# Optimization experiments

Measured on AMD Instinct MI355X. Metric: run time of the kernel, lower is better.

The kernel has to match this reference:

```python
import jax, jax.numpy as jnp
import numpy as np

K = 2            # negative:positive edge ratio (init arg k)
N_NODES = 4096
N_EDGES = 8192
FEAT = 64


def setup_inputs() -> dict:
    key = jax.random.key(0)
    k1, k2, k3 = jax.random.split(key, 3)
    node_feature = jax.random.normal(k1, (N_NODES, FEAT), dtype=jnp.float32)
    edge_src = jax.random.randint(k2, (N_EDGES,), 0, N_NODES, dtype=jnp.int32)
    edge_dst = jax.random.randint(k3, (N_EDGES,), 0, N_NODES, dtype=jnp.int32)
    return {"node_feature": node_feature, "edge_src": edge_src, "edge_dst": edge_dst}


def reference(node_feature, edge_src, edge_dst):
    E = edge_src.shape[0]
    N = node_feature.shape[0]
    # [E, E] pairwise mask: candidate column j is valid for row i iff
    # dst[j] != dst[i] and dst[j] != src[i]
    valid = (edge_dst[:, None] != edge_dst[None, :]) & (edge_src[:, None] != edge_dst[None, :])
    # unsorted_segment_min over rows grouped by edge_src -> [N, E]
    segmin = jax.ops.segment_min(valid.astype(jnp.int8), edge_src, num_segments=N)
    # gather back per edge -> [E, E], flatten
    m = segmin[edge_src].reshape(-1).astype(bool)  # [E*E]
    num_negatives = jnp.sum(m)
    ratio = num_negatives // E                      # integer ratio as in TF code
    keep_prob = (K / ratio).astype(jnp.float32)
    u = jax.random.uniform(jax.random.key(42), (E * E,), dtype=jnp.float32)
    keep = m & (u < keep_prob)
    # fixed-size (jit-friendly) stand-in for tf.boolean_mask: expected count is K*E;
    # pad/truncate to exactly K*E kept flat indices (fill_value=0 pads).
    idx = jnp.nonzero(keep, size=K * E, fill_value=0)[0]
    rows = idx // E
    cols = idx % E
    edge_src_neg = edge_src[rows]
    edge_dst_neg = edge_dst[cols]
    return edge_src_neg, edge_dst_neg
```

## Files before the change

kernel.cpp:

```cpp
#include <hip/hip_runtime.h>
#include <stdint.h>

typedef unsigned int u32;
typedef unsigned long long u64;

#define E_CNT   8192
#define N_CNT   4096
#define TOT_N   (1u << 26)
#define OUT_K   16384
#define NODE_BM_WORDS 128
#define N_CHUNKS 1024

#define OFF_BAD      0x000000
#define OFF_CNT_DST  0x200000
#define OFF_CNT_SRC  0x204000
#define OFF_CCOUNT   0x208000
#define OFF_COFF     0x209000
#define OFF_SCALARS  0x20A000
#define OFF_KEEPBM   0x210000
#define ZERO_BYTES   0x20A100

__device__ __forceinline__ u32 rotl32(u32 x, u32 d) { return (x << d) | (x >> (32u - d)); }

__device__ __forceinline__ void threefry_0_42(u32 x0, u32 x1, u32& o0, u32& o1) {
  const u32 k0 = 0u, k1 = 42u, k2 = 0x1BD11BF0u;
  x0 += k0; x1 += k1;
#define TF_R(r) { x0 += x1; x1 = rotl32(x1, r); x1 ^= x0; }
  TF_R(13) TF_R(15) TF_R(26) TF_R(6)
  x0 += k1; x1 += k2 + 1u;
  TF_R(17) TF_R(29) TF_R(16) TF_R(24)
  x0 += k2; x1 += k0 + 2u;
  TF_R(13) TF_R(15) TF_R(26) TF_R(6)
  x0 += k0; x1 += k1 + 3u;
  TF_R(17) TF_R(29) TF_R(16) TF_R(24)
  x0 += k1; x1 += k2 + 4u;
  TF_R(13) TF_R(15) TF_R(26) TF_R(6)
  x0 += k2; x1 += k0 + 5u;
#undef TF_R
  o0 = x0; o1 = x1;
}

__device__ __forceinline__ float bits_to_unif(u32 b) {
  return __uint_as_float((b >> 9) | 0x3f800000u) - 1.0f;
}

__global__ void k_build(const int* __restrict__ src, const int* __restrict__ dst,
                        u32* __restrict__ bad, u32* __restrict__ cnt_dst,
                        u32* __restrict__ cnt_src) {
  int tid = blockIdx.x * 256 + threadIdx.x;
  if (tid < N_CNT) {
    atomicOr(&bad[(u32)tid * NODE_BM_WORDS + ((u32)tid >> 5)], 1u << (tid & 31));
  }
  if (tid < E_CNT) {
    u32 s = (u32)src[tid], d = (u32)dst[tid];
    atomicOr(&bad[s * NODE_BM_WORDS + (d >> 5)], 1u << (d & 31));
    atomicAdd(&cnt_dst[d], 1u);
    atomicAdd(&cnt_src[s], 1u);
  }
}

__global__ void k_rowcount(const u32* __restrict__ bad, const u32* __restrict__ cnt_dst,
                           const u32* __restrict__ cnt_src, u32* __restrict__ num_neg) {
  int n = blockIdx.x * 256 + threadIdx.x;
  u32 sum = 0;
  const u32* row = bad + (u32)n * NODE_BM_WORDS;
  for (int w = 0; w < NODE_BM_WORDS; ++w) {
    u32 bits = row[w];
    while (bits) { int b = __ffs(bits) - 1; sum += cnt_dst[w * 32 + b]; bits &= bits - 1; }
  }
  u32 contrib = ((u32)E_CNT - sum) * cnt_src[n];
  __shared__ u32 red[256];
  red[threadIdx.x] = contrib; __syncthreads();
  for (int off = 128; off > 0; off >>= 1) {
    if (threadIdx.x < off) red[threadIdx.x] += red[threadIdx.x + off];
    __syncthreads();
  }
  if (threadIdx.x == 0) atomicAdd(num_neg, red[0]);
}

__global__ void k_prob(const u32* __restrict__ num_neg, float* __restrict__ kp) {
  u32 ratio = num_neg[0] / (u32)E_CNT;
  kp[0] = 2.0f / (float)ratio;
}

__global__ void __launch_bounds__(256) k_sample(const int* __restrict__ src,
                                                const int* __restrict__ dst,
                                                const u32* __restrict__ bad,
                                                const float* __restrict__ kp_p,
                                                u64* __restrict__ keep_bm,
                                                u32* __restrict__ ccount) {
  u32 i = blockIdx.x * 256u + threadIdx.x;
  u32 o0, o1;
  threefry_0_42(0u, i, o0, o1);
  float u = bits_to_unif(o0 ^ o1);
  float kp = kp_p[0];
  bool keep = u < kp;
  if (keep) {
    u32 n = (u32)src[i >> 13]; u32 v = (u32)dst[i & 8191];
    keep = ((bad[n * NODE_BM_WORDS + (v >> 5)] >> (v & 31)) & 1u) == 0u;
  }
  u64 m = __ballot(keep);
  if ((threadIdx.x & 63) == 0) {
    keep_bm[i >> 6] = m;
    if (m) atomicAdd(&ccount[i >> 16], (u32)__popcll(m));
  }
}

__global__ void k_scan(const u32* __restrict__ ccount, u32* __restrict__ coff) {
  __shared__ u32 s[N_CHUNKS];
  int t = threadIdx.x;
  u32 mine = ccount[t];
  s[t] = mine; __syncthreads();
  for (int off = 1; off < N_CHUNKS; off <<= 1) {
    u32 v = (t >= off) ? s[t - off] : 0u;
    __syncthreads();
    s[t] += v;
    __syncthreads();
  }
  coff[t] = s[t] - mine;
}

__global__ void k_prefill(const int* __restrict__ src, const int* __restrict__ dst,
                          int* __restrict__ out) {
  int r = blockIdx.x * 256 + threadIdx.x;
  out[r] = src[0];
  out[OUT_K + r] = dst[0];
}

__global__ void k_compact(const int* __restrict__ src, const int* __restrict__ dst,
                          const u64* __restrict__ keep_bm, const u32* __restrict__ coff,
                          int* __restrict__ out) {
  int c = blockIdx.x;
  const u64* words = keep_bm + (size_t)c * 1024;
  int t = threadIdx.x;
  u64 w[4];
  u32 cnt = 0;
#pragma unroll
  for (int k = 0; k < 4; ++k) { w[k] = words[4 * t + k]; cnt += (u32)__popcll(w[k]); }
  __shared__ u32 s[256];
  s[t] = cnt; __syncthreads();
  for (int off = 1; off < 256; off <<= 1) {
    u32 v = (t >= off) ? s[t - off] : 0u;
    __syncthreads();
    s[t] += v;
    __syncthreads();
  }
  u32 rank = coff[c] + s[t] - cnt;
  u32 tbase = (u32)c * 65536u + (u32)t * 256u;
#pragma unroll
  for (int k = 0; k < 4; ++k) {
    u64 bits = w[k];
    while (bits) {
      int b = __ffsll((unsigned long long)bits) - 1;
      if (rank < OUT_K) {
        u32 tt = tbase + (u32)k * 64u + (u32)b;
        out[rank]         = src[tt >> 13];
        out[OUT_K + rank] = dst[tt & 8191];
      }
      rank++;
      bits &= bits - 1;
    }
  }
}

extern "C" void kernel_launch(void* const* d_in, const int* in_sizes, int n_in,
                              void* d_out, int out_size, void* d_ws, size_t ws_size,
                              hipStream_t stream) {
  const int* src = (const int*)d_in[1];
  const int* dst = (const int*)d_in[2];
  int* out = (int*)d_out;
  char* ws = (char*)d_ws;

  u32*   bad     = (u32*)(ws + OFF_BAD);
  u32*   cnt_dst = (u32*)(ws + OFF_CNT_DST);
  u32*   cnt_src = (u32*)(ws + OFF_CNT_SRC);
  u32*   ccount  = (u32*)(ws + OFF_CCOUNT);
  u32*   coff    = (u32*)(ws + OFF_COFF);
  u32*   num_neg = (u32*)(ws + OFF_SCALARS);
  float* kp      = (float*)(ws + OFF_SCALARS + 4);
  u64*   keep_bm = (u64*)(ws + OFF_KEEPBM);

  hipMemsetAsync(ws, 0, ZERO_BYTES, stream);
  k_build<<<(E_CNT + 255) / 256, 256, 0, stream>>>(src, dst, bad, cnt_dst, cnt_src);
  k_rowcount<<<N_CNT / 256, 256, 0, stream>>>(bad, cnt_dst, cnt_src, num_neg);
  k_prob<<<1, 1, 0, stream>>>(num_neg, kp);
  k_sample<<<TOT_N / 256, 256, 0, stream>>>(src, dst, bad, kp, keep_bm, ccount);
  k_scan<<<1, N_CHUNKS, 0, stream>>>(ccount, coff);
  k_prefill<<<OUT_K / 256, 256, 0, stream>>>(src, dst, out);
  k_compact<<<N_CHUNKS, 256, 0, stream>>>(src, dst, keep_bm, coff, out);
}
```

Before: 228.1 us.

## Fuse small kernels: prefill into build, prob into rowcount, scan into compact

Cuts the launch chain from seven kernels to four. The output prefill now happens in k_build, and the keep-probability is computed by the last block of k_rowcount through a completion counter. Each k_compact block redoes the 1024-chunk prefix scan redundantly. k_rowcount now uses one wavefront per node with a shuffle reduction, and k_sample compares integer random bits against a precomputed threshold instead of converting to float. These changes remove launch gaps and tiny serial kernels, at the cost of redundant scan work and relying on the threshold comparison being exactly equivalent to the float one.

```diff
diff --git a/kernel.cpp b/kernel.cpp
--- a/kernel.cpp
+++ b/kernel.cpp
@@ -1,5 +1,6 @@
 #include <hip/hip_runtime.h>
 #include <stdint.h>
+#include <math.h>
 
 typedef unsigned int u32;
 typedef unsigned long long u64;
@@ -15,10 +16,9 @@
 #define OFF_CNT_DST  0x200000
 #define OFF_CNT_SRC  0x204000
 #define OFF_CCOUNT   0x208000
-#define OFF_COFF     0x209000
-#define OFF_SCALARS  0x20A000
+#define OFF_SCALARS  0x209000
 #define OFF_KEEPBM   0x210000
-#define ZERO_BYTES   0x20A100
+#define ZERO_BYTES   0x209040
 
 __device__ __forceinline__ u32 rotl32(u32 x, u32 d) { return (x << d) | (x >> (32u - d)); }
 
@@ -40,61 +40,61 @@
   o0 = x0; o1 = x1;
 }
 
-__device__ __forceinline__ float bits_to_unif(u32 b) {
-  return __uint_as_float((b >> 9) | 0x3f800000u) - 1.0f;
-}
-
 __global__ void k_build(const int* __restrict__ src, const int* __restrict__ dst,
                         u32* __restrict__ bad, u32* __restrict__ cnt_dst,
-                        u32* __restrict__ cnt_src) {
+                        u32* __restrict__ cnt_src, int* __restrict__ out) {
   int tid = blockIdx.x * 256 + threadIdx.x;
   if (tid < N_CNT) {
     atomicOr(&bad[(u32)tid * NODE_BM_WORDS + ((u32)tid >> 5)], 1u << (tid & 31));
   }
-  if (tid < E_CNT) {
-    u32 s = (u32)src[tid], d = (u32)dst[tid];
-    atomicOr(&bad[s * NODE_BM_WORDS + (d >> 5)], 1u << (d & 31));
-    atomicAdd(&cnt_dst[d], 1u);
-    atomicAdd(&cnt_src[s], 1u);
-  }
+  u32 s = (u32)src[tid], d = (u32)dst[tid];
+  atomicOr(&bad[s * NODE_BM_WORDS + (d >> 5)], 1u << (d & 31));
+  atomicAdd(&cnt_dst[d], 1u);
+  atomicAdd(&cnt_src[s], 1u);
+  int s0 = src[0], d0 = dst[0];
+  out[tid] = s0;            out[tid + E_CNT] = s0;
+  out[OUT_K + tid] = d0;    out[OUT_K + tid + E_CNT] = d0;
 }
 
 __global__ void k_rowcount(const u32* __restrict__ bad, const u32* __restrict__ cnt_dst,
-                           const u32* __restrict__ cnt_src, u32* __restrict__ num_neg) {
-  int n = blockIdx.x * 256 + threadIdx.x;
+                           const u32* __restrict__ cnt_src, u32* __restrict__ scal) {
+  int n = blockIdx.x * 4 + (threadIdx.x >> 6);
+  int l = threadIdx.x & 63;
+  const u32* row = bad + (u32)n * NODE_BM_WORDS;
   u32 sum = 0;
-  const u32* row = bad + (u32)n * NODE_BM_WORDS;
-  for (int w = 0; w < NODE_BM_WORDS; ++w) {
+#pragma unroll
+  for (int h = 0; h < 2; ++h) {
+    int w = l + h * 64;
     u32 bits = row[w];
-    while (bits) { int b = __ffs(bits) - 1; sum += cnt_dst[w * 32 + b]; bits &= bits - 1; }
+    while (bits) { int b = __ffs(bits) - 1; sum += cnt_dst[(w << 5) + b]; bits &= bits - 1; }
   }
-  u32 contrib = ((u32)E_CNT - sum) * cnt_src[n];
-  __shared__ u32 red[256];
-  red[threadIdx.x] = contrib; __syncthreads();
-  for (int off = 128; off > 0; off >>= 1) {
-    if (threadIdx.x < off) red[threadIdx.x] += red[threadIdx.x + off];
-    __syncthreads();
+#pragma unroll
+  for (int off = 32; off > 0; off >>= 1) sum += __shfl_down(sum, off, 64);
+  if (l == 0) atomicAdd(&scal[0], ((u32)E_CNT - sum) * cnt_src[n]);
+  __syncthreads();
+  if (threadIdx.x == 0) {
+    __threadfence();
+    if (atomicAdd(&scal[1], 1u) == (u32)(N_CNT / 4 - 1)) {
+      u32 nn = atomicAdd(&scal[0], 0u);
+      u32 ratio = nn >> 13;
+      float kp = 2.0f / (float)ratio;
+      u32 T = (u32)ceil((double)kp * 8388608.0);
+      atomicExch(&scal[2], T);
+    }
   }
-  if (threadIdx.x == 0) atomicAdd(num_neg, red[0]);
-}
-
-__global__ void k_prob(const u32* __restrict__ num_neg, float* __restrict__ kp) {
-  u32 ratio = num_neg[0] / (u32)E_CNT;
-  kp[0] = 2.0f / (float)ratio;
 }
 
 __global__ void __launch_bounds__(256) k_sample(const int* __restrict__ src,
                                                 const int* __restrict__ dst,
                                                 const u32* __restrict__ bad,
-                                                const float* __restrict__ kp_p,
+                                                const u32* __restrict__ scal,
                                                 u64* __restrict__ keep_bm,
                                                 u32* __restrict__ ccount) {
   u32 i = blockIdx.x * 256u + threadIdx.x;
   u32 o0, o1;
   threefry_0_42(0u, i, o0, o1);
-  float u = bits_to_unif(o0 ^ o1);
-  float kp = kp_p[0];
-  bool keep = u < kp;
+  u32 T = scal[2];
+  bool keep = ((o0 ^ o1) >> 9) < T;
   if (keep) {
     u32 n = (u32)src[i >> 13]; u32 v = (u32)dst[i & 8191];
     keep = ((bad[n * NODE_BM_WORDS + (v >> 5)] >> (v & 31)) & 1u) == 0u;
@@ -106,46 +106,47 @@
   }
 }
 
-__global__ void k_scan(const u32* __restrict__ ccount, u32* __restrict__ coff) {
-  __shared__ u32 s[N_CHUNKS];
+__global__ void k_compact(const int* __restrict__ src, const int* __restrict__ dst,
+                          const u64* __restrict__ keep_bm, const u32* __restrict__ ccount,
+                          int* __restrict__ out) {
+  int c = blockIdx.x;
   int t = threadIdx.x;
-  u32 mine = ccount[t];
-  s[t] = mine; __syncthreads();
-  for (int off = 1; off < N_CHUNKS; off <<= 1) {
-    u32 v = (t >= off) ? s[t - off] : 0u;
+  __shared__ u32 s[256];
+  __shared__ u32 base_sh;
+
+  u32 v[4]; u32 sum4 = 0;
+#pragma unroll
+  for (int k = 0; k < 4; ++k) { v[k] = ccount[4 * t + k]; sum4 += v[k]; }
+  s[t] = sum4; __syncthreads();
+  for (int off = 1; off < 256; off <<= 1) {
+    u32 x = (t >= off) ? s[t - off] : 0u;
     __syncthreads();
-    s[t] += v;
+    s[t] += x;
     __syncthreads();
   }
-  coff[t] = s[t] - mine;
-}
+  if (t == (c >> 2)) {
+    u32 excl = s[t] - sum4;
+#pragma unroll
+    for (int k = 0; k < 4; ++k) if (k < (c & 3)) excl += v[k];
+    base_sh = excl;
+  }
+  __syncthreads();
+  u32 coff_c = base_sh;
+  __syncthreads();
 
-__global__ void k_prefill(const int* __restrict__ src, const int* __restrict__ dst,
-                          int* __restrict__ out) {
-  int r = blockIdx.x * 256 + threadIdx.x;
-  out[r] = src[0];
-  out[OUT_K + r] = dst[0];
-}
-
-__global__ void k_compact(const int* __restrict__ src, const int* __restrict__ dst,
-                          const u64* __restrict__ keep_bm, const u32* __restrict__ coff,
-                          int* __restrict__ out) {
-  int c = blockIdx.x;
   const u64* words = keep_bm + (size_t)c * 1024;
-  int t = threadIdx.x;
   u64 w[4];
   u32 cnt = 0;
 #pragma unroll
   for (int k = 0; k < 4; ++k) { w[k] = words[4 * t + k]; cnt += (u32)__popcll(w[k]); }
-  __shared__ u32 s[256];
   s[t] = cnt; __syncthreads();
   for (int off = 1; off < 256; off <<= 1) {
-    u32 v = (t >= off) ? s[t - off] : 0u;
+    u32 x = (t >= off) ? s[t - off] : 0u;
     __syncthreads();
-    s[t] += v;
+    s[t] += x;
     __syncthreads();
   }
-  u32 rank = coff[c] + s[t] - cnt;
+  u32 rank = coff_c + s[t] - cnt;
   u32 tbase = (u32)c * 65536u + (u32)t * 256u;
 #pragma unroll
   for (int k = 0; k < 4; ++k) {
@@ -171,21 +172,16 @@
   int* out = (int*)d_out;
   char* ws = (char*)d_ws;
 
-  u32*   bad     = (u32*)(ws + OFF_BAD);
-  u32*   cnt_dst = (u32*)(ws + OFF_CNT_DST);
-  u32*   cnt_src = (u32*)(ws + OFF_CNT_SRC);
-  u32*   ccount  = (u32*)(ws + OFF_CCOUNT);
-  u32*   coff    = (u32*)(ws + OFF_COFF);
-  u32*   num_neg = (u32*)(ws + OFF_SCALARS);
-  float* kp      = (float*)(ws + OFF_SCALARS + 4);
-  u64*   keep_bm = (u64*)(ws + OFF_KEEPBM);
+  u32* bad     = (u32*)(ws + OFF_BAD);
+  u32* cnt_dst = (u32*)(ws + OFF_CNT_DST);
+  u32* cnt_src = (u32*)(ws + OFF_CNT_SRC);
+  u32* ccount  = (u32*)(ws + OFF_CCOUNT);
+  u32* scal    = (u32*)(ws + OFF_SCALARS);
+  u64* keep_bm = (u64*)(ws + OFF_KEEPBM);
 
   hipMemsetAsync(ws, 0, ZERO_BYTES, stream);
-  k_build<<<(E_CNT + 255) / 256, 256, 0, stream>>>(src, dst, bad, cnt_dst, cnt_src);
-  k_rowcount<<<N_CNT / 256, 256, 0, stream>>>(bad, cnt_dst, cnt_src, num_neg);
-  k_prob<<<1, 1, 0, stream>>>(num_neg, kp);
-  k_sample<<<TOT_N / 256, 256, 0, stream>>>(src, dst, bad, kp, keep_bm, ccount);
-  k_scan<<<1, N_CHUNKS, 0, stream>>>(ccount, coff);
-  k_prefill<<<OUT_K / 256, 256, 0, stream>>>(src, dst, out);
-  k_compact<<<N_CHUNKS, 256, 0, stream>>>(src, dst, keep_bm, coff, out);
+  k_build<<<E_CNT / 256, 256, 0, stream>>>(src, dst, bad, cnt_dst, cnt_src, out);
+  k_rowcount<<<N_CNT / 4, 256, 0, stream>>>(bad, cnt_dst, cnt_src, scal);
+  k_sample<<<TOT_N / 256, 256, 0, stream>>>(src, dst, bad, scal, keep_bm, ccount);
+  k_compact<<<N_CHUNKS, 256, 0, stream>>>(src, dst, keep_bm, ccount, out);
 }
```

New measurement: 248.8 us. +9.1%, slower.
